# Performance work log

Hardware: AMD Instinct MI355X
Metric: run time of the kernel (lower is better)

## Reference

```python
import jax, jax.numpy as jnp
import numpy as np

HIDDEN = 768
HEADS = 12
HEAD_DIM = HIDDEN // HEADS


def setup_inputs() -> dict:
    key = jax.random.key(0)
    ks = jax.random.split(key, 9)
    B, S = 2, 2048
    scale = 1.0 / np.sqrt(HIDDEN)
    return {
        "hidden_states": jax.random.normal(ks[0], (B, S, HIDDEN), jnp.float32),
        "context": jax.random.normal(ks[1], (B, S, HIDDEN), jnp.float32),
        "attention_mask": jnp.zeros((B, 1, 1, S), jnp.float32),
        "Wq": jax.random.normal(ks[2], (HIDDEN, HIDDEN), jnp.float32) * scale,
        "bq": jnp.zeros((HIDDEN,), jnp.float32),
        "Wk": jax.random.normal(ks[3], (HIDDEN, HIDDEN), jnp.float32) * scale,
        "bk": jnp.zeros((HIDDEN,), jnp.float32),
        "Wv": jax.random.normal(ks[4], (HIDDEN, HIDDEN), jnp.float32) * scale,
        "bv": jnp.zeros((HIDDEN,), jnp.float32),
    }


def _split_heads(x):
    # [B, S, H*D] -> [B, H, S, D]
    B, S, _ = x.shape
    return x.reshape(B, S, HEADS, HEAD_DIM).transpose(0, 2, 1, 3)


def reference(hidden_states, context, attention_mask, Wq, bq, Wk, bk, Wv, bv):
    # torch Linear: y = x @ W^T + b
    q = _split_heads(hidden_states @ Wq.T + bq)   # [B,H,Sq,D]
    k = _split_heads(context @ Wk.T + bk)         # [B,H,Sk,D]
    v = _split_heads(context @ Wv.T + bv)         # [B,H,Sk,D]

    scores = jnp.einsum("bhqd,bhkd->bhqk", q, k)
    scores = scores / np.sqrt(HEAD_DIM + 1e-05)
    scores = scores + attention_mask
    probs = jax.nn.softmax(scores, axis=-1)       # dropout p=0 -> identity (eval)
    ctx = jnp.einsum("bhqk,bhkd->bhqd", probs, v) # [B,H,Sq,D]
    B, H, Sq, D = ctx.shape
    return ctx.transpose(0, 2, 1, 3).reshape(B, Sq, H * D)
```

## Files before the change

kernel.cpp:

```cpp
#include <hip/hip_runtime.h>
#include <hip/hip_bf16.h>
#include <math.h>

typedef short s16x8 __attribute__((ext_vector_type(8)));
typedef float f32x4 __attribute__((ext_vector_type(4)));
typedef _Float16 f16x4 __attribute__((ext_vector_type(4)));
typedef __fp16 fp16x2 __attribute__((ext_vector_type(2)));
typedef unsigned short u16;

#define NHEADS 12
#define SEQ 2048
#define NBH 24
#define KDIM 768
#define NSPL 2
#define LOG2E 1.44269504088896f

#define SWZ(row, col) (((row) * 64) + ((col) ^ (((row) & 7) << 3)))

#define GLOAD_LDS16(g, l) __builtin_amdgcn_global_load_lds( \
    (const __attribute__((address_space(1))) unsigned int*)(g), \
    (__attribute__((address_space(3))) unsigned int*)(l), 16, 0, 0)

static __device__ __forceinline__ u16 f2bf(float f) {
    union { float f; unsigned u; } v; v.f = f;
    unsigned r = v.u + 0x7fffu + ((v.u >> 16) & 1u);
    return (u16)(r >> 16);
}
static __device__ __forceinline__ u16 f2h(float f) {
    union { _Float16 h; u16 u; } v; v.h = (_Float16)f;
    return v.u;
}
static __device__ __forceinline__ f16x4 pack4(float a, float b, float c, float d) {
    union { fp16x2 h2[2]; f16x4 h4; } u;
    u.h2[0] = __builtin_amdgcn_cvt_pkrtz(a, b);
    u.h2[1] = __builtin_amdgcn_cvt_pkrtz(c, d);
    return u.h4;
}

#define CVT_O1 786432
#define CVT_O2 1572864
#define CVT_O3 1720320
#define CVT_O4 1867776
#define CVT_O5 2015232
#define CVT_TOT 2016256
__global__ void cvt1d_kernel(const float* __restrict__ s0, const float* __restrict__ s1,
                             const float* __restrict__ s2, const float* __restrict__ s3,
                             const float* __restrict__ s4, const float* __restrict__ s5,
                             u16* __restrict__ d0, u16* __restrict__ d1, u16* __restrict__ d2,
                             u16* __restrict__ d3, u16* __restrict__ d4, float* __restrict__ d5,
                             float qscl) {
    int i = blockIdx.x * 256 + threadIdx.x;
    if (i >= CVT_TOT) return;
    if (i >= CVT_O5) {
        int j = i - CVT_O5;
        float4 f = ((const float4*)s5)[j];
        f.x *= LOG2E; f.y *= LOG2E; f.z *= LOG2E; f.w *= LOG2E;
        ((float4*)d5)[j] = f;
        return;
    }
    const float* src; u16* dst; int off; float scl = 1.0f;
    if (i < CVT_O1)      { src = s0; dst = d0; off = 0; }
    else if (i < CVT_O2) { src = s1; dst = d1; off = CVT_O1; }
    else if (i < CVT_O3) { src = s2; dst = d2; off = CVT_O2; scl = qscl; }
    else if (i < CVT_O4) { src = s3; dst = d3; off = CVT_O3; }
    else                 { src = s4; dst = d4; off = CVT_O4; }
    int j = i - off;
    float4 f = ((const float4*)src)[j];
    ushort4 o;
    o.x = f2bf(f.x * scl); o.y = f2bf(f.y * scl); o.z = f2bf(f.z * scl); o.w = f2bf(f.w * scl);
    ((ushort4*)dst)[j] = o;
}

__launch_bounds__(256)
__global__ void qkv_gemm(const u16* __restrict__ X, const u16* __restrict__ C,
                         const u16* __restrict__ W0, const u16* __restrict__ W1, const u16* __restrict__ W2,
                         const float* __restrict__ b0, const float* __restrict__ b1, const float* __restrict__ b2,
                         u16* __restrict__ Qo, u16* __restrict__ Ko, u16* __restrict__ Vo, float qscl) {
    const int z = blockIdx.z;
    const u16* A    = (z == 0) ? X  : C;
    const u16* W    = (z == 0) ? W0 : (z == 1) ? W1 : W2;
    const float* bi = (z == 0) ? b0 : (z == 1) ? b1 : b2;
    u16* out        = (z == 0) ? Qo : (z == 1) ? Ko : Vo;
    const float bscl = (z == 0) ? qscl : 1.0f;

    __shared__ u16 As[3][4096];
    __shared__ u16 Bs[3][4096];

    const int tid  = threadIdx.x;
    const int lane = tid & 63;
    const int wid  = tid >> 6;
    const int wr = wid >> 1, wc = wid & 1;
    const int l15 = lane & 15, lh = lane >> 4;
    const int mBase = blockIdx.x * 128;
    const int nBase = blockIdx.y * 128;

    size_t aSrc[2], bSrc[2]; int ldsOff[2];
    #pragma unroll
    for (int i = 0; i < 2; ++i) {
        int L = i * 2048 + tid * 8;
        int prow = L >> 6;
        int pcol = (L & 63) ^ ((prow & 7) << 3);
        int row = (prow << 1) | (pcol >> 5);
        int col = pcol & 31;
        aSrc[i] = (size_t)(mBase + row) * KDIM + col;
        bSrc[i] = (size_t)(nBase + row) * KDIM + col;
        ldsOff[i] = i * 2048 + wid * 512;
    }

#define G_STAGE(step, buf) do { \
        const size_t kb_ = (size_t)(step) * 32; \
        GLOAD_LDS16(&A[aSrc[0] + kb_], &As[buf][ldsOff[0]]); \
        GLOAD_LDS16(&A[aSrc[1] + kb_], &As[buf][ldsOff[1]]); \
        GLOAD_LDS16(&W[bSrc[0] + kb_], &Bs[buf][ldsOff[0]]); \
        GLOAD_LDS16(&W[bSrc[1] + kb_], &Bs[buf][ldsOff[1]]); \
    } while (0)

    f32x4 acc[4][4] = {};

    G_STAGE(0, 0);
    G_STAGE(1, 1);

    const int NIT = KDIM / 32;
    int cur = 0;
    for (int it = 0; it < NIT; ++it) {
        if (it + 1 < NIT) asm volatile("s_waitcnt vmcnt(4)" ::: "memory");
        else              asm volatile("s_waitcnt vmcnt(0)" ::: "memory");
        __builtin_amdgcn_s_barrier();
        __builtin_amdgcn_sched_barrier(0);

        s16x8 xf[4], wf[4];
        #pragma unroll
        for (int m = 0; m < 4; ++m) {
            int row = wr * 64 + m * 16 + l15;
            xf[m] = *(const s16x8*)(&As[cur][SWZ(row >> 1, (row & 1) * 32 + lh * 8)]);
        }
        #pragma unroll
        for (int n = 0; n < 4; ++n) {
            int row = wc * 64 + n * 16 + l15;
            wf[n] = *(const s16x8*)(&Bs[cur][SWZ(row >> 1, (row & 1) * 32 + lh * 8)]);
        }
        if (z < 2) {
            #pragma unroll
            for (int m = 0; m < 4; ++m)
                #pragma unroll
                for (int n = 0; n < 4; ++n)
                    acc[m][n] = __builtin_amdgcn_mfma_f32_16x16x32_bf16(wf[n], xf[m], acc[m][n], 0, 0, 0);
        } else {
            #pragma unroll
            for (int m = 0; m < 4; ++m)
                #pragma unroll
                for (int n = 0; n < 4; ++n)
                    acc[m][n] = __builtin_amdgcn_mfma_f32_16x16x32_bf16(xf[m], wf[n], acc[m][n], 0, 0, 0);
        }

        if (it + 2 < NIT) {
            int nxt = cur + 2; if (nxt >= 3) nxt -= 3;
            G_STAGE(it + 2, nxt);
        }
        ++cur; if (cur == 3) cur = 0;
    }
#undef G_STAGE

    if (z < 2) {
        #pragma unroll
        for (int m = 0; m < 4; ++m) {
            int sg = mBase + wr * 64 + m * 16 + l15;
            int b = sg >> 11, s = sg & 2047;
            #pragma unroll
            for (int n = 0; n < 4; ++n) {
                int d0 = nBase + wc * 64 + n * 16 + lh * 4;
                int h = d0 >> 6, d = d0 & 63;
                float4 bv = *(const float4*)(&bi[d0]);
                ushort4 o;
                o.x = f2bf(acc[m][n][0] + bv.x * bscl);
                o.y = f2bf(acc[m][n][1] + bv.y * bscl);
                o.z = f2bf(acc[m][n][2] + bv.z * bscl);
                o.w = f2bf(acc[m][n][3] + bv.w * bscl);
                *(ushort4*)(&out[(((size_t)(b * NHEADS + h) * SEQ + s) << 6) + d]) = o;
            }
        }
    } else {
        #pragma unroll
        for (int m = 0; m < 4; ++m) {
            #pragma unroll
            for (int n = 0; n < 4; ++n) {
                int colg = nBase + wc * 64 + n * 16 + l15;
                float bv = bi[colg];
                int h = colg >> 6, d = colg & 63;
                int rowg0 = mBase + wr * 64 + m * 16 + lh * 4;
                int b = rowg0 >> 11, s = rowg0 & 2047;
                int sp = (s & ~0x3C) | (((s >> 2) & 3) << 4) | (((s >> 4) & 3) << 2);
                ushort4 o;
                o.x = f2h(acc[m][n][0] + bv);
                o.y = f2h(acc[m][n][1] + bv);
                o.z = f2h(acc[m][n][2] + bv);
                o.w = f2h(acc[m][n][3] + bv);
                *(ushort4*)(&out[(((size_t)(b * NHEADS + h) * 64 + d) << 11) + sp]) = o;
            }
        }
    }
}

template<int NSPLIT>
__launch_bounds__(512)
__global__ void attn_kernel(const u16* __restrict__ Qg, const u16* __restrict__ Kg,
                            const u16* __restrict__ Vg,
                            const float* __restrict__ maskL, float* __restrict__ out,
                            u16* __restrict__ OpartH, float* __restrict__ MLpart) {
    constexpr int NT = SEQ / 64 / NSPLIT;
    __shared__ u16 Ks[3][4096];
    __shared__ u16 Vt[3][4096];
    __shared__ float maskLds[NT * 64];

    const int tid  = threadIdx.x;
    const int lane = tid & 63;
    const int wid  = tid >> 6;

    int qx, bh, z;
    if (NSPLIT == 2) {
        int L = blockIdx.x + 16 * (blockIdx.y + NBH * blockIdx.z);
        int xcd = L & 7, idx = L >> 3;
        int grp = xcd * 6 + (idx >> 4);
        qx = idx & 15;
        bh = grp % NBH;
        z  = grp / NBH;
    } else {
        qx = blockIdx.x; bh = blockIdx.y; z = 0;
    }
    const int b = bh / NHEADS;
    const int h = bh % NHEADS;
    const int q0 = qx * 128 + wid * 16;
    const int l15 = lane & 15, lh = lane >> 4;
    const int tile0 = z * NT;

    for (int i = tid * 4; i < NT * 64; i += 512 * 4)
        *(float4*)(&maskLds[i]) = *(const float4*)(&maskL[(size_t)b * SEQ + (tile0 << 6) + i]);
    asm volatile("s_waitcnt lgkmcnt(0)" ::: "memory");

    const int srow = tid >> 3;
    const int scol = ((tid & 7) * 8) ^ ((srow & 7) << 3);
    const size_t kSrc = (((size_t)bh * SEQ + srow) << 6) + scol + ((size_t)tile0 << 12);
    const size_t vSrc = (((size_t)bh * 64 + srow) << 11) + scol + (size_t)tile0 * 64;
    const int ldsBase = wid * 512;

#define A_STAGE(t, buf) do { \
        GLOAD_LDS16(&Kg[kSrc + ((size_t)(t) << 12)], &Ks[buf][ldsBase]); \
        GLOAD_LDS16(&Vg[vSrc + (size_t)(t) * 64],    &Vt[buf][ldsBase]); \
    } while (0)

    s16x8 qf[2];
    #pragma unroll
    for (int kk = 0; kk < 2; ++kk)
        qf[kk] = *(const s16x8*)(&Qg[(((size_t)bh * SEQ + q0 + l15) << 6) + kk * 32 + lh * 8]);

    f32x4 oacc[4] = {};
    f32x4 lacc0 = {}, lacc1 = {};
    const f16x4 onesA = {(_Float16)1.0f, (_Float16)1.0f, (_Float16)1.0f, (_Float16)1.0f};
    float mrun = -1e30f;

    A_STAGE(0, 0);
    A_STAGE(1, 1);

    int cur = 0;
    for (int t = 0; t < NT; ++t) {
        if (t + 1 < NT) asm volatile("s_waitcnt vmcnt(2)" ::: "memory");
        else            asm volatile("s_waitcnt vmcnt(0)" ::: "memory");
        __builtin_amdgcn_s_barrier();
        __builtin_amdgcn_sched_barrier(0);

        if (t + 2 < NT) {
            int nxt = cur + 2; if (nxt >= 3) nxt -= 3;
            A_STAGE(t + 2, nxt);
        }

        f32x4 sacc[4];
        #pragma unroll
        for (int n = 0; n < 4; ++n) {
            float4 mv = *(const float4*)(&maskLds[t * 64 + n * 16 + lh * 4]);
            sacc[n][0] = mv.x; sacc[n][1] = mv.y; sacc[n][2] = mv.z; sacc[n][3] = mv.w;
        }
        __builtin_amdgcn_s_setprio(1);
        #pragma unroll
        for (int kk = 0; kk < 2; ++kk) {
            #pragma unroll
            for (int n = 0; n < 4; ++n) {
                s16x8 kf = *(const s16x8*)(&Ks[cur][SWZ(n * 16 + l15, kk * 32 + lh * 8)]);
                sacc[n] = __builtin_amdgcn_mfma_f32_16x16x32_bf16(kf, qf[kk], sacc[n], 0, 0, 0);
            }
        }
        __builtin_amdgcn_s_setprio(0);

        float t0 = fmaxf(fmaxf(sacc[0][0], sacc[0][1]), sacc[0][2]);
        float t1 = fmaxf(fmaxf(sacc[0][3], sacc[1][0]), sacc[1][1]);
        float t2 = fmaxf(fmaxf(sacc[1][2], sacc[1][3]), sacc[2][0]);
        float t3 = fmaxf(fmaxf(sacc[2][1], sacc[2][2]), sacc[2][3]);
        float t4 = fmaxf(fmaxf(sacc[3][0], sacc[3][1]), sacc[3][2]);
        float tmax = fmaxf(fmaxf(fmaxf(t0, t1), t2), fmaxf(fmaxf(t3, t4), sacc[3][3]));

        if (!__all(tmax - mrun <= 11.0f)) {
            float rmax = fmaxf(tmax, __shfl_xor(tmax, 16));
            rmax = fmaxf(rmax, __shfl_xor(rmax, 32));
            float mnew = fmaxf(mrun, rmax);
            float alpha = __builtin_amdgcn_exp2f(mrun - mnew);
            #pragma unroll
            for (int j = 0; j < 4; ++j) { lacc0[j] *= alpha; lacc1[j] *= alpha; }
            #pragma unroll
            for (int nd = 0; nd < 4; ++nd)
                #pragma unroll
                for (int j = 0; j < 4; ++j)
                    oacc[nd][j] *= alpha;
            mrun = mnew;
        }

        f16x4 pf[4];
        #pragma unroll
        for (int n = 0; n < 4; ++n) {
            float p0 = __builtin_amdgcn_exp2f(sacc[n][0] - mrun);
            float p1 = __builtin_amdgcn_exp2f(sacc[n][1] - mrun);
            float p2 = __builtin_amdgcn_exp2f(sacc[n][2] - mrun);
            float p3 = __builtin_amdgcn_exp2f(sacc[n][3] - mrun);
            pf[n] = pack4(p0, p1, p2, p3);
        }

        __builtin_amdgcn_s_setprio(1);
        lacc0 = __builtin_amdgcn_mfma_f32_16x16x16f16(onesA, pf[0], lacc0, 0, 0, 0);
        lacc1 = __builtin_amdgcn_mfma_f32_16x16x16f16(onesA, pf[1], lacc1, 0, 0, 0);
        lacc0 = __builtin_amdgcn_mfma_f32_16x16x16f16(onesA, pf[2], lacc0, 0, 0, 0);
        lacc1 = __builtin_amdgcn_mfma_f32_16x16x16f16(onesA, pf[3], lacc1, 0, 0, 0);
        #pragma unroll
        for (int kk = 0; kk < 2; ++kk) {
            #pragma unroll
            for (int nd = 0; nd < 4; ++nd) {
                s16x8 v2 = *(const s16x8*)(&Vt[cur][SWZ(nd * 16 + l15, lh * 16 + kk * 8)]);
                union { s16x8 s8; f16x4 h4[2]; } u; u.s8 = v2;
                oacc[nd] = __builtin_amdgcn_mfma_f32_16x16x16f16(u.h4[0], pf[2 * kk],     oacc[nd], 0, 0, 0);
                oacc[nd] = __builtin_amdgcn_mfma_f32_16x16x16f16(u.h4[1], pf[2 * kk + 1], oacc[nd], 0, 0, 0);
            }
        }
        __builtin_amdgcn_s_setprio(0);

        ++cur; if (cur == 3) cur = 0;
    }
#undef A_STAGE

    const float lrun = lacc0[0] + lacc1[0];
    const float inv = 1.0f / lrun;
    const int s = q0 + l15;
    if (NSPLIT == 1) {
        #pragma unroll
        for (int nd = 0; nd < 4; ++nd) {
            float4 o;
            o.x = oacc[nd][0] * inv; o.y = oacc[nd][1] * inv;
            o.z = oacc[nd][2] * inv; o.w = oacc[nd][3] * inv;
            *(float4*)(&out[(size_t)(b * SEQ + s) * (NHEADS * 64) + h * 64 + nd * 16 + lh * 4]) = o;
        }
    } else {
        const size_t rbase = ((size_t)(z * NBH + bh) * SEQ + s);
        #pragma unroll
        for (int nd = 0; nd < 4; ++nd) {
            union { f16x4 h4; ushort4 u4; } o;
            o.h4 = pack4(oacc[nd][0] * inv, oacc[nd][1] * inv,
                         oacc[nd][2] * inv, oacc[nd][3] * inv);
            *(ushort4*)(&OpartH[rbase * 64 + nd * 16 + lh * 4]) = o.u4;
        }
        if (lh == 0)
            *(float2*)(&MLpart[rbase * 2]) = make_float2(mrun, lrun);
    }
}

__global__ void combine_kernel(const u16* __restrict__ OpartH, const float* __restrict__ MLpart,
                               float* __restrict__ out) {
    int gid = blockIdx.x * 256 + threadIdx.x;
    int row = gid >> 4, d4 = gid & 15;
    float2 ml[NSPL];
    float m = -1e30f;
    #pragma unroll
    for (int k = 0; k < NSPL; ++k) {
        ml[k] = ((const float2*)MLpart)[(size_t)k * NBH * SEQ + row];
        m = fmaxf(m, ml[k].x);
    }
    float w[NSPL], wsum = 0.f;
    #pragma unroll
    for (int k = 0; k < NSPL; ++k) {
        w[k] = __builtin_amdgcn_exp2f(ml[k].x - m) * ml[k].y;
        wsum += w[k];
    }
    float inv = 1.0f / wsum;
    float4 o = {0.f, 0.f, 0.f, 0.f};
    #pragma unroll
    for (int k = 0; k < NSPL; ++k) {
        union { ushort4 u4; f16x4 h4; } a;
        a.u4 = *(const ushort4*)(&OpartH[((size_t)k * NBH * SEQ + row) * 64 + d4 * 4]);
        float wk = w[k] * inv;
        o.x += (float)a.h4[0] * wk; o.y += (float)a.h4[1] * wk;
        o.z += (float)a.h4[2] * wk; o.w += (float)a.h4[3] * wk;
    }
    int bh = row >> 11, s = row & 2047;
    int b = bh / NHEADS, hh = bh % NHEADS;
    *(float4*)(&out[(size_t)(b * SEQ + s) * (NHEADS * 64) + hh * 64 + d4 * 4]) = o;
}

extern "C" void kernel_launch(void* const* d_in, const int* in_sizes, int n_in,
                              void* d_out, int out_size, void* d_ws, size_t ws_size,
                              hipStream_t stream) {
    const float* hidden  = (const float*)d_in[0];
    const float* context = (const float*)d_in[1];
    const float* mask    = (const float*)d_in[2];
    const float* Wq = (const float*)d_in[3];
    const float* bq = (const float*)d_in[4];
    const float* Wk = (const float*)d_in[5];
    const float* bk = (const float*)d_in[6];
    const float* Wv = (const float*)d_in[7];
    const float* bv = (const float*)d_in[8];
    float* out = (float*)d_out;

    char* ws = (char*)d_ws;
    const size_t XSZ = (size_t)4096 * 768 * 2;
    const size_t WSZ = (size_t)768 * 768 * 2;
    u16* X16  = (u16*)(ws);
    u16* C16  = (u16*)(ws + XSZ);
    u16* W16q = (u16*)(ws + 2 * XSZ);
    u16* W16k = (u16*)(ws + 2 * XSZ + WSZ);
    u16* W16v = (u16*)(ws + 2 * XSZ + 2 * WSZ);
    u16* Q16  = (u16*)(ws + 2 * XSZ + 3 * WSZ);
    u16* K16  = (u16*)(ws + 3 * XSZ + 3 * WSZ);
    u16* V16  = (u16*)(ws + 4 * XSZ + 3 * WSZ);
    const size_t MASKL_OFF = 5 * XSZ + 3 * WSZ;
    float* maskL = (float*)(ws + MASKL_OFF);
    const size_t OPART_OFF = MASKL_OFF + 2 * SEQ * sizeof(float) + 256;
    u16* OpartH = (u16*)(ws + OPART_OFF);
    const size_t ML_OFF = OPART_OFF + (size_t)NSPL * NBH * SEQ * 64 * 2;
    float* MLpart = (float*)(ws + ML_OFF);
    const size_t WS_NEED_SPLIT = ML_OFF + (size_t)NSPL * NBH * SEQ * 2 * 4;

    const float qscl = (float)((1.0 / sqrt(64.0 + 1e-5)) * 1.44269504088896);

    cvt1d_kernel<<<(CVT_TOT + 255) / 256, 256, 0, stream>>>(
        hidden, context, Wq, Wk, Wv, mask,
        X16, C16, W16q, W16k, W16v, maskL, qscl);

    qkv_gemm<<<dim3(4096 / 128, 768 / 128, 3), 256, 0, stream>>>(
        X16, C16, W16q, W16k, W16v, bq, bk, bv, Q16, K16, V16, qscl);

    if (ws_size >= WS_NEED_SPLIT) {
        attn_kernel<NSPL><<<dim3(SEQ / 128, NBH, NSPL), 512, 0, stream>>>(
            Q16, K16, V16, maskL, out, OpartH, MLpart);
        combine_kernel<<<(NBH * SEQ * 16) / 256, 256, 0, stream>>>(OpartH, MLpart, out);
    } else {
        attn_kernel<1><<<dim3(SEQ / 128, NBH, 1), 512, 0, stream>>>(
            Q16, K16, V16, maskL, out, OpartH, MLpart);
    }
}
```

Before: 95.44 us.

## Software-pipeline QK of next tile with softmax and PV of previous tile

Restructures the attention loop into a two-stage software pipeline. The QK^T MFMAs for tile t are issued while the softmax and PV for tile t-1 run, alternating between two score accumulators. V fragments are copied into registers right after each barrier, so the triple-buffered LDS slot can be refilled safely. The row sum is now built with scalar adds plus a final cross-lane shuffle instead of extra ones-matrix MFMAs, trading MFMA work for VALU work. The loop is hard-unrolled for 16 tiles, which adds register pressure and ties the code to that tile count.

```diff
diff --git a/kernel.cpp b/kernel.cpp
--- a/kernel.cpp
+++ b/kernel.cpp
@@ -254,96 +254,128 @@
         qf[kk] = *(const s16x8*)(&Qg[(((size_t)bh * SEQ + q0 + l15) << 6) + kk * 32 + lh * 8]);
 
     f32x4 oacc[4] = {};
-    f32x4 lacc0 = {}, lacc1 = {};
-    const f16x4 onesA = {(_Float16)1.0f, (_Float16)1.0f, (_Float16)1.0f, (_Float16)1.0f};
-    float mrun = -1e30f;
+    f32x4 saccA[4], saccB[4];
+    s16x8 vreg[8];
+    float mrun = -1e30f, lrun = 0.f;
 
     A_STAGE(0, 0);
     A_STAGE(1, 1);
 
-    int cur = 0;
-    for (int t = 0; t < NT; ++t) {
-        if (t + 1 < NT) asm volatile("s_waitcnt vmcnt(2)" ::: "memory");
-        else            asm volatile("s_waitcnt vmcnt(0)" ::: "memory");
+#define QK(SC, t) do { \
+        const int buf_ = (t) % 3; \
+        _Pragma("unroll") \
+        for (int n = 0; n < 4; ++n) { \
+            float4 mv = *(const float4*)(&maskLds[(t) * 64 + n * 16 + lh * 4]); \
+            SC[n][0] = mv.x; SC[n][1] = mv.y; SC[n][2] = mv.z; SC[n][3] = mv.w; \
+        } \
+        __builtin_amdgcn_s_setprio(1); \
+        _Pragma("unroll") \
+        for (int kk = 0; kk < 2; ++kk) { \
+            _Pragma("unroll") \
+            for (int n = 0; n < 4; ++n) { \
+                s16x8 kf = *(const s16x8*)(&Ks[buf_][SWZ(n * 16 + l15, kk * 32 + lh * 8)]); \
+                SC[n] = __builtin_amdgcn_mfma_f32_16x16x32_bf16(kf, qf[kk], SC[n], 0, 0, 0); \
+            } \
+        } \
+        __builtin_amdgcn_s_setprio(0); \
+    } while (0)
+
+#define SM_PV(SP) do { \
+        float t0 = fmaxf(fmaxf(SP[0][0], SP[0][1]), SP[0][2]); \
+        float t1 = fmaxf(fmaxf(SP[0][3], SP[1][0]), SP[1][1]); \
+        float t2 = fmaxf(fmaxf(SP[1][2], SP[1][3]), SP[2][0]); \
+        float t3 = fmaxf(fmaxf(SP[2][1], SP[2][2]), SP[2][3]); \
+        float t4 = fmaxf(fmaxf(SP[3][0], SP[3][1]), SP[3][2]); \
+        float tmax = fmaxf(fmaxf(fmaxf(t0, t1), t2), fmaxf(fmaxf(t3, t4), SP[3][3])); \
+        if (!__all(tmax - mrun <= 11.0f)) { \
+            float rmax = fmaxf(tmax, __shfl_xor(tmax, 16)); \
+            rmax = fmaxf(rmax, __shfl_xor(rmax, 32)); \
+            float mnew = fmaxf(mrun, rmax); \
+            float alpha = __builtin_amdgcn_exp2f(mrun - mnew); \
+            lrun *= alpha; \
+            _Pragma("unroll") \
+            for (int nd = 0; nd < 4; ++nd) \
+                _Pragma("unroll") \
+                for (int j = 0; j < 4; ++j) \
+                    oacc[nd][j] *= alpha; \
+            mrun = mnew; \
+        } \
+        f16x4 pf[4]; \
+        _Pragma("unroll") \
+        for (int n = 0; n < 4; ++n) { \
+            float p0 = __builtin_amdgcn_exp2f(SP[n][0] - mrun); \
+            float p1 = __builtin_amdgcn_exp2f(SP[n][1] - mrun); \
+            float p2 = __builtin_amdgcn_exp2f(SP[n][2] - mrun); \
+            float p3 = __builtin_amdgcn_exp2f(SP[n][3] - mrun); \
+            lrun += (p0 + p1) + (p2 + p3); \
+            pf[n] = pack4(p0, p1, p2, p3); \
+        } \
+        __builtin_amdgcn_s_setprio(1); \
+        _Pragma("unroll") \
+        for (int kk = 0; kk < 2; ++kk) { \
+            _Pragma("unroll") \
+            for (int nd = 0; nd < 4; ++nd) { \
+                union { s16x8 s8; f16x4 h4[2]; } u; u.s8 = vreg[kk * 4 + nd]; \
+                oacc[nd] = __builtin_amdgcn_mfma_f32_16x16x16f16(u.h4[0], pf[2 * kk],     oacc[nd], 0, 0, 0); \
+                oacc[nd] = __builtin_amdgcn_mfma_f32_16x16x16f16(u.h4[1], pf[2 * kk + 1], oacc[nd], 0, 0, 0); \
+            } \
+        } \
+        __builtin_amdgcn_s_setprio(0); \
+    } while (0)
+
+#define VLOAD(t) do { \
+        const int buf_ = (t) % 3; \
+        _Pragma("unroll") \
+        for (int kk = 0; kk < 2; ++kk) \
+            _Pragma("unroll") \
+            for (int nd = 0; nd < 4; ++nd) \
+                vreg[kk * 4 + nd] = *(const s16x8*)(&Vt[buf_][SWZ(nd * 16 + l15, lh * 16 + kk * 8)]); \
+    } while (0)
+
+    asm volatile("s_waitcnt vmcnt(2)" ::: "memory");
+    __builtin_amdgcn_s_barrier();
+    __builtin_amdgcn_sched_barrier(0);
+    A_STAGE(2, 2);
+    QK(saccA, 0);
+    VLOAD(0);
+
+    for (int tp = 0; tp < 7; ++tp) {
+        int t = 2 * tp + 1;
+        asm volatile("s_waitcnt vmcnt(2)" ::: "memory");
         __builtin_amdgcn_s_barrier();
         __builtin_amdgcn_sched_barrier(0);
-
-        if (t + 2 < NT) {
-            int nxt = cur + 2; if (nxt >= 3) nxt -= 3;
-            A_STAGE(t + 2, nxt);
-        }
-
-        f32x4 sacc[4];
-        #pragma unroll
-        for (int n = 0; n < 4; ++n) {
-            float4 mv = *(const float4*)(&maskLds[t * 64 + n * 16 + lh * 4]);
-            sacc[n][0] = mv.x; sacc[n][1] = mv.y; sacc[n][2] = mv.z; sacc[n][3] = mv.w;
-        }
-        __builtin_amdgcn_s_setprio(1);
-        #pragma unroll
-        for (int kk = 0; kk < 2; ++kk) {
-            #pragma unroll
-            for (int n = 0; n < 4; ++n) {
-                s16x8 kf = *(const s16x8*)(&Ks[cur][SWZ(n * 16 + l15, kk * 32 + lh * 8)]);
-                sacc[n] = __builtin_amdgcn_mfma_f32_16x16x32_bf16(kf, qf[kk], sacc[n], 0, 0, 0);
-            }
-        }
-        __builtin_amdgcn_s_setprio(0);
-
-        float t0 = fmaxf(fmaxf(sacc[0][0], sacc[0][1]), sacc[0][2]);
-        float t1 = fmaxf(fmaxf(sacc[0][3], sacc[1][0]), sacc[1][1]);
-        float t2 = fmaxf(fmaxf(sacc[1][2], sacc[1][3]), sacc[2][0]);
-        float t3 = fmaxf(fmaxf(sacc[2][1], sacc[2][2]), sacc[2][3]);
-        float t4 = fmaxf(fmaxf(sacc[3][0], sacc[3][1]), sacc[3][2]);
-        float tmax = fmaxf(fmaxf(fmaxf(t0, t1), t2), fmaxf(fmaxf(t3, t4), sacc[3][3]));
-
-        if (!__all(tmax - mrun <= 11.0f)) {
-            float rmax = fmaxf(tmax, __shfl_xor(tmax, 16));
-            rmax = fmaxf(rmax, __shfl_xor(rmax, 32));
-            float mnew = fmaxf(mrun, rmax);
-            float alpha = __builtin_amdgcn_exp2f(mrun - mnew);
-            #pragma unroll
-            for (int j = 0; j < 4; ++j) { lacc0[j] *= alpha; lacc1[j] *= alpha; }
-            #pragma unroll
-            for (int nd = 0; nd < 4; ++nd)
-                #pragma unroll
-                for (int j = 0; j < 4; ++j)
-                    oacc[nd][j] *= alpha;
-            mrun = mnew;
-        }
-
-        f16x4 pf[4];
-        #pragma unroll
-        for (int n = 0; n < 4; ++n) {
-            float p0 = __builtin_amdgcn_exp2f(sacc[n][0] - mrun);
-            float p1 = __builtin_amdgcn_exp2f(sacc[n][1] - mrun);
-            float p2 = __builtin_amdgcn_exp2f(sacc[n][2] - mrun);
-            float p3 = __builtin_amdgcn_exp2f(sacc[n][3] - mrun);
-            pf[n] = pack4(p0, p1, p2, p3);
-        }
-
-        __builtin_amdgcn_s_setprio(1);
-        lacc0 = __builtin_amdgcn_mfma_f32_16x16x16f16(onesA, pf[0], lacc0, 0, 0, 0);
-        lacc1 = __builtin_amdgcn_mfma_f32_16x16x16f16(onesA, pf[1], lacc1, 0, 0, 0);
-        lacc0 = __builtin_amdgcn_mfma_f32_16x16x16f16(onesA, pf[2], lacc0, 0, 0, 0);
-        lacc1 = __builtin_amdgcn_mfma_f32_16x16x16f16(onesA, pf[3], lacc1, 0, 0, 0);
-        #pragma unroll
-        for (int kk = 0; kk < 2; ++kk) {
-            #pragma unroll
-            for (int nd = 0; nd < 4; ++nd) {
-                s16x8 v2 = *(const s16x8*)(&Vt[cur][SWZ(nd * 16 + l15, lh * 16 + kk * 8)]);
-                union { s16x8 s8; f16x4 h4[2]; } u; u.s8 = v2;
-                oacc[nd] = __builtin_amdgcn_mfma_f32_16x16x16f16(u.h4[0], pf[2 * kk],     oacc[nd], 0, 0, 0);
-                oacc[nd] = __builtin_amdgcn_mfma_f32_16x16x16f16(u.h4[1], pf[2 * kk + 1], oacc[nd], 0, 0, 0);
-            }
-        }
-        __builtin_amdgcn_s_setprio(0);
-
-        ++cur; if (cur == 3) cur = 0;
-    }
+        if (t + 2 < NT) { int nb = (t + 2) % 3; A_STAGE(t + 2, nb); }
+        QK(saccB, t);
+        SM_PV(saccA);
+        VLOAD(t);
+
+        t = 2 * tp + 2;
+        asm volatile("s_waitcnt vmcnt(2)" ::: "memory");
+        __builtin_amdgcn_s_barrier();
+        __builtin_amdgcn_sched_barrier(0);
+        if (t + 2 < NT) { int nb = (t + 2) % 3; A_STAGE(t + 2, nb); }
+        QK(saccA, t);
+        SM_PV(saccB);
+        VLOAD(t);
+    }
+
+    asm volatile("s_waitcnt vmcnt(0)" ::: "memory");
+    __builtin_amdgcn_s_barrier();
+    __builtin_amdgcn_sched_barrier(0);
+    QK(saccB, 15);
+    SM_PV(saccA);
+    VLOAD(15);
+
+    SM_PV(saccB);
+
+#undef QK
+#undef SM_PV
+#undef VLOAD
 #undef A_STAGE
 
-    const float lrun = lacc0[0] + lacc1[0];
+    lrun += __shfl_xor(lrun, 16);
+    lrun += __shfl_xor(lrun, 32);
+
     const float inv = 1.0f / lrun;
     const int s = q0 + l15;
     if (NSPLIT == 1) {
```

New measurement: 110.1 us. 15.4% more time.
